# Performance work log

Hardware: AMD Instinct MI355X
Metric: run time of the kernel (lower is better)

## Reference

```python
import jax, jax.numpy as jnp
import numpy as np

N_NODES = 50000
N_EDGES = 800000
EMB = 128      # embedding_dim
GH1 = 128      # gn_hidden_dim1
GH2 = 128      # gn_hidden_dim2
LH = 256       # lstm_hidden_dim
AH = 128       # answer_hidden_dim
AD = 1         # answer_dim
NQ = 512       # number of questions (len(sentence_idx_list))
NS = NQ * 4    # total sentences
MAXLEN = 32    # padded sentence length


def setup_inputs() -> dict:
    key = jax.random.key(0)
    ks = jax.random.split(key, 16)
    s = 0.05
    inputs = jax.random.normal(ks[0], (N_NODES, EMB), jnp.float32)
    src = jax.random.randint(ks[1], (N_EDGES,), 0, N_NODES)
    dst = jax.random.randint(ks[2], (N_EDGES,), 0, N_NODES)
    sentence_idx = jax.random.randint(ks[3], (NS, MAXLEN), 0, N_NODES)
    lengths = jax.random.randint(ks[4], (NS,), 1, MAXLEN + 1)
    # GCN linear layers (torch nn.Linear convention: y = x @ W.T + b)
    W1 = jax.random.normal(ks[5], (GH1, EMB), jnp.float32) * s
    b1 = jnp.zeros((GH1,), jnp.float32)
    W2 = jax.random.normal(ks[6], (GH2, GH1), jnp.float32) * s
    b2 = jnp.zeros((GH2,), jnp.float32)
    # LSTM params (gate order i,f,g,o as in torch)
    Wi = jax.random.normal(ks[7], (4 * LH, GH2), jnp.float32) * s
    Wh = jax.random.normal(ks[8], (4 * LH, LH), jnp.float32) * s
    bi = jnp.zeros((4 * LH,), jnp.float32)
    bh = jnp.zeros((4 * LH,), jnp.float32)
    # sentence_classifier
    Wc1 = jax.random.normal(ks[9], (AH, LH), jnp.float32) * s
    bc1 = jnp.zeros((AH,), jnp.float32)
    Wc2 = jax.random.normal(ks[10], (AD, AH), jnp.float32) * s
    bc2 = jnp.zeros((AD,), jnp.float32)
    return dict(inputs=inputs, W1=W1, b1=b1, W2=W2, b2=b2,
                Wi=Wi, Wh=Wh, bi=bi, bh=bh,
                Wc1=Wc1, bc1=bc1, Wc2=Wc2, bc2=bc2,
                src=src, dst=dst, sentence_idx=sentence_idx, lengths=lengths)


def reference(inputs, W1, b1, W2, b2, Wi, Wh, bi, bh, Wc1, bc1, Wc2, bc2,
              src, dst, sentence_idx, lengths):
    # --- GCN: sum-aggregate over edges, then linear; tanh between layers ---
    agg1 = jax.ops.segment_sum(inputs[src], dst, num_segments=N_NODES)  # [N, EMB]
    h = jnp.tanh(agg1 @ W1.T + b1)                                      # [N, GH1]
    agg2 = jax.ops.segment_sum(h[src], dst, num_segments=N_NODES)       # [N, GH1]
    hn = agg2 @ W2.T + b2                                               # [N, GH2]

    # --- Batched ragged LSTM over all sentences (padded to MAXLEN) ---
    x = hn[sentence_idx]                  # [NS, MAXLEN, GH2]
    x = jnp.swapaxes(x, 0, 1)             # [MAXLEN, NS, GH2] (time-major)

    def step(carry, xt):
        hp, cp = carry
        gates = xt @ Wi.T + bi + hp @ Wh.T + bh            # [NS, 4*LH]
        i, f, g, o = jnp.split(gates, 4, axis=-1)
        c = jax.nn.sigmoid(f) * cp + jax.nn.sigmoid(i) * jnp.tanh(g)
        hcur = jax.nn.sigmoid(o) * jnp.tanh(c)
        return (hcur, c), hcur

    h0 = jnp.zeros((NS, LH), x.dtype)
    c0 = jnp.zeros((NS, LH), x.dtype)
    _, hs = jax.lax.scan(step, (h0, c0), x)                # [MAXLEN, NS, LH]
    h_last = hs[lengths - 1, jnp.arange(NS)]               # [NS, LH] (hn at true seq end)

    # relu then sentence_classifier (linear-relu-linear)
    e = jax.nn.relu(h_last)
    sc = jax.nn.relu(e @ Wc1.T + bc1) @ Wc2.T + bc2        # [NS, 1]
    return sc.reshape(NQ, 4)
```

## Files before the change

kernel.cpp:

```cpp
#include <hip/hip_runtime.h>
#include <hip/hip_bf16.h>
#include <math.h>

#define N_NODES 50000
#define N_EDGES 800000
#define EMB 128
#define LH 256
#define NSENT 2048
#define MAXLEN 32
#define SCAN_NB 196
#define NG 64
#define NGRP 32

typedef __attribute__((ext_vector_type(8))) short short8;
typedef __attribute__((ext_vector_type(4))) float f32x4;

__device__ __forceinline__ unsigned short f2bf_u(float f) {
    __hip_bfloat16 h = __float2bfloat16(f);
    return *reinterpret_cast<unsigned short*>(&h);
}
__device__ __forceinline__ float bfu2f(unsigned short u) {
    unsigned int x = ((unsigned int)u) << 16;
    return __uint_as_float(x);
}

__device__ __forceinline__ float fsig(float x) {
    return 1.f / (1.f + __expf(-x));
}
__device__ __forceinline__ float ftanh(float x) {
    return 1.f - 2.f / (__expf(2.f * x) + 1.f);
}

#define WAITVM0() __builtin_amdgcn_s_waitcnt(0xF70)

__device__ __forceinline__ void gload_lds16(const void* gsrc, void* ldst) {
    __builtin_amdgcn_global_load_lds(
        (const __attribute__((address_space(1))) unsigned int*)gsrc,
        (__attribute__((address_space(3))) unsigned int*)ldst, 16, 0, 0);
}


__global__ void k_hist(const int* __restrict__ dst, int* __restrict__ cnt) {
    int i = blockIdx.x * 256 + threadIdx.x;
    if (i < N_EDGES) atomicAdd(&cnt[dst[i]], 1);
}

__global__ void k_scan_blk(const int* __restrict__ cnt, int* __restrict__ row_ptr,
                           int* __restrict__ blk) {
    int b = blockIdx.x, t = threadIdx.x;
    int i = b * 256 + t;
    int lane = t & 63, wid = t >> 6;
    int v = (i < N_NODES) ? cnt[i] : 0;
    int x = v;
    #pragma unroll
    for (int off = 1; off < 64; off <<= 1) {
        int y = __shfl_up(x, off);
        if (lane >= off) x += y;
    }
    __shared__ int ws[4];
    if (lane == 63) ws[wid] = x;
    __syncthreads();
    if (t == 0) {
        int s = 0;
        #pragma unroll
        for (int j = 0; j < 4; j++) { int tmp = ws[j]; ws[j] = s; s += tmp; }
        blk[b] = s;
    }
    __syncthreads();
    if (i < N_NODES) row_ptr[i] = ws[wid] + x - v;
}

__global__ void k_scan_tot(int* __restrict__ blk) {
    int t = threadIdx.x;
    int lane = t & 63, wid = t >> 6;
    int v = (t < SCAN_NB) ? blk[t] : 0;
    int x = v;
    #pragma unroll
    for (int off = 1; off < 64; off <<= 1) {
        int y = __shfl_up(x, off);
        if (lane >= off) x += y;
    }
    __shared__ int ws[4];
    if (lane == 63) ws[wid] = x;
    __syncthreads();
    if (t == 0) {
        int s = 0;
        #pragma unroll
        for (int j = 0; j < 4; j++) { int tmp = ws[j]; ws[j] = s; s += tmp; }
    }
    __syncthreads();
    if (t < SCAN_NB) blk[t] = ws[wid] + x - v;
}

__global__ void k_scan_add(int* __restrict__ row_ptr, const int* __restrict__ blk) {
    int i = blockIdx.x * 256 + threadIdx.x;
    if (i < N_NODES) row_ptr[i] += blk[i >> 8];
    if (i == 0) row_ptr[N_NODES] = N_EDGES;
}

__global__ void k_scatter(const int* __restrict__ src, const int* __restrict__ dst,
                          const int* __restrict__ row_ptr, int* __restrict__ cnt,
                          int* __restrict__ edge_src) {
    int i = blockIdx.x * 256 + threadIdx.x;
    if (i < N_EDGES) {
        int d = dst[i];
        int pos = row_ptr[d] + atomicAdd(&cnt[d], 1);
        edge_src[pos] = src[i];
    }
}


__global__ void k_tobf16(const float* __restrict__ x, unsigned short* __restrict__ y) {
    int i = blockIdx.x * 256 + threadIdx.x;
    float4 v = ((const float4*)x)[i];
    ushort4 u;
    u.x = f2bf_u(v.x); u.y = f2bf_u(v.y); u.z = f2bf_u(v.z); u.w = f2bf_u(v.w);
    ((ushort4*)y)[i] = u;
}


__global__ void k_aggregate_bf(const unsigned short* __restrict__ feat,
                               const int* __restrict__ row_ptr,
                               const int* __restrict__ edge_src,
                               unsigned short* __restrict__ outb) {
    int w = (blockIdx.x * 256 + threadIdx.x) >> 6;
    int lane = threadIdx.x & 63;
    if (w >= N_NODES) return;
    int slot = lane >> 4, li = lane & 15;
    int beg = row_ptr[w], end = row_ptr[w + 1];
    float acc[8] = {};
    short8 vA = {}, vB = {};
    {
        int eA = beg + slot, eB = beg + 4 + slot;
        int sA = (eA < end) ? edge_src[eA] : -1;
        int sB = (eB < end) ? edge_src[eB] : -1;
        if (sA >= 0) vA = *(const short8*)((const short*)feat + (size_t)sA * EMB + li * 8);
        if (sB >= 0) vB = *(const short8*)((const short*)feat + (size_t)sB * EMB + li * 8);
    }
    #pragma unroll 1
    for (int e = beg; e < end; e += 8) {
        int eA2 = e + 8 + slot, eB2 = e + 12 + slot;
        int sA2 = (eA2 < end) ? edge_src[eA2] : -1;
        int sB2 = (eB2 < end) ? edge_src[eB2] : -1;
        short8 vA2 = {}, vB2 = {};
        if (sA2 >= 0) vA2 = *(const short8*)((const short*)feat + (size_t)sA2 * EMB + li * 8);
        if (sB2 >= 0) vB2 = *(const short8*)((const short*)feat + (size_t)sB2 * EMB + li * 8);
        if (e + slot < end) {
            #pragma unroll
            for (int j = 0; j < 8; j++) acc[j] += bfu2f((unsigned short)vA[j]);
        }
        if (e + 4 + slot < end) {
            #pragma unroll
            for (int j = 0; j < 8; j++) acc[j] += bfu2f((unsigned short)vB[j]);
        }
        vA = vA2; vB = vB2;
    }
    #pragma unroll
    for (int j = 0; j < 8; j++) {
        float t = acc[j];
        t += __shfl_xor(t, 16);
        t += __shfl_xor(t, 32);
        acc[j] = t;
    }
    if (slot == 0) {
        short8 o;
        #pragma unroll
        for (int j = 0; j < 8; j++) o[j] = (short)f2bf_u(acc[j]);
        *(short8*)((short*)outb + (size_t)w * EMB + li * 8) = o;
    }
}


__global__ void __launch_bounds__(256)
k_gcn_mfma(const unsigned short* __restrict__ Ab,
           const unsigned short* __restrict__ Wb,
           const float* __restrict__ bias,
           unsigned short* __restrict__ outb,
           int M, int do_tanh) {
    int tid = threadIdx.x;
    int w = tid >> 6, lane = tid & 63;
    int l16 = lane & 15, quad = lane >> 4;
    int rbase = blockIdx.x * 64 + w * 16;
    int arow = rbase + l16;
    if (arow >= M) arow = M - 1;
    const short* Ap = (const short*)Ab + (size_t)arow * 128 + quad * 8;
    const short* Wp = (const short*)Wb;
    f32x4 acc[8] = {};
    #pragma unroll
    for (int ks = 0; ks < 4; ks++) {
        short8 a = *(const short8*)(Ap + ks * 32);
        #pragma unroll
        for (int ct = 0; ct < 8; ct++) {
            short8 b = *(const short8*)(Wp + (size_t)(ct * 16 + l16) * 128 + ks * 32 + quad * 8);
            acc[ct] = __builtin_amdgcn_mfma_f32_16x16x32_bf16(a, b, acc[ct], 0, 0, 0);
        }
    }
    #pragma unroll
    for (int ct = 0; ct < 8; ct++) {
        float bcol = bias[ct * 16 + l16];
        #pragma unroll
        for (int r = 0; r < 4; r++) {
            int row = rbase + quad * 4 + r;
            if (row < M) {
                float v = acc[ct][r] + bcol;
                if (do_tanh) v = tanhf(v);
                outb[(size_t)row * 128 + ct * 16 + l16] = f2bf_u(v);
            }
        }
    }
}


__global__ void k_prep(const float* __restrict__ Wi, const float* __restrict__ Wh,
                       const float* __restrict__ bi, const float* __restrict__ bh,
                       const float* __restrict__ W1, const float* __restrict__ W2,
                       unsigned short* __restrict__ Wpk3, float* __restrict__ bsum,
                       unsigned short* __restrict__ W1b, unsigned short* __restrict__ W2b) {
    int idx = blockIdx.x * 256 + threadIdx.x;
    if (idx < 1024 * 384) {
        int R = idx / 384, k = idx - R * 384;
        float v = (k < 128) ? Wi[R * 128 + k] : Wh[R * 256 + (k - 128)];
        int g = R >> 8, u = R & 255;
        int usl = u >> 5, up = u & 31;
        int ct = g * 2 + (up >> 4);
        int l16v = up & 15;
        int ks = k >> 5, kk = k & 31;
        int quad = kk >> 3, jj = kk & 7;
        int lane = quad * 16 + l16v;
        Wpk3[(((size_t)usl * 12 + ks) * 8 + ct) * 512 + lane * 8 + jj] = f2bf_u(v);
    } else if (idx < 1024 * 384 + 1024) {
        int r = idx - 1024 * 384;
        bsum[r] = bi[r] + bh[r];
    } else if (idx < 1024 * 384 + 1024 + 16384) {
        int r = idx - (1024 * 384 + 1024);
        W1b[r] = f2bf_u(W1[r]);
    } else if (idx < 1024 * 384 + 1024 + 32768) {
        int r = idx - (1024 * 384 + 1024 + 16384);
        W2b[r] = f2bf_u(W2[r]);
    }
}


__global__ void __launch_bounds__(512)
__attribute__((amdgpu_waves_per_eu(2, 2)))
k_lstm_ws8(const unsigned short* __restrict__ hn_bf,
           const unsigned short* __restrict__ Wpk3,
           const float* __restrict__ bsum,
           const int* __restrict__ sidx,
           const int* __restrict__ lengths,
           unsigned long long* __restrict__ hX,
           int* __restrict__ gcnt,
           float* __restrict__ h_last) {
    __shared__ unsigned short xb[64 * 128];
    __shared__ unsigned short hb[64 * 256];
    __shared__ float gl[64 * 132];
    __shared__ int nid_sh[NG * 33];

    int tid = threadIdx.x;
    int w = tid >> 6, lane = tid & 63;
    int l16 = lane & 15, quad = lane >> 4;
    int usl = blockIdx.x >> 5;
    int grp = blockIdx.x & 31;
    int s0 = grp * NG;
    const short* hnp = (const short*)hn_bf;

    int m2 = w >> 2, cp4 = w & 3;
    int row0 = m2 * 32 + l16, row1 = row0 + 16;

    short8 breg[12][2];
    {
        const short* wsrc = (const short*)Wpk3 + (size_t)usl * 49152 + lane * 8;
        #pragma unroll
        for (int ks = 0; ks < 12; ks++)
            #pragma unroll
            for (int c = 0; c < 2; c++)
                breg[ks][c] = *(const short8*)(wsrc + (size_t)(ks * 8 + cp4 * 2 + c) * 512);
    }
    float bc0 = bsum[cp4 * 256 + usl * 32 + l16];
    float bc1 = bsum[cp4 * 256 + usl * 32 + 16 + l16];

    #pragma unroll
    for (int i = 0; i < 2; i++) {
        int row = w * 8 + i * 4 + quad;
        int nid = sidx[(size_t)(s0 + row) * MAXLEN + 0];
        int schunk = (l16 & ~7) | ((l16 ^ row) & 7);
        gload_lds16(hnp + (size_t)nid * 128 + schunk * 8,
                    (void*)((char*)xb + (size_t)(w * 8 + i * 4) * 256));
    }
    for (int i = tid; i < NG * 32; i += 512)
        nid_sh[(i >> 5) * 33 + (i & 31)] = sidx[(size_t)(s0 + (i >> 5)) * MAXLEN + (i & 31)];
    for (int i = tid; i < 64 * 128; i += 512) ((unsigned int*)hb)[i] = 0;

    int psent = tid >> 3, j8 = tid & 7, u0 = j8 * 4;
    int len_reg = lengths[s0 + psent];
    float c_reg[4] = {};

    short8 xr[2];

    __syncthreads();

    #pragma unroll 1
    for (int t = 0; t < MAXLEN; t++) {
        if (t + 1 < MAXLEN) {
            int row = tid >> 3;
            int nid = nid_sh[row * 33 + (t + 1)];
            #pragma unroll
            for (int k = 0; k < 2; k++) {
                int slot = j8 * 2 + k;
                int c = (slot & ~7) | ((slot ^ row) & 7);
                xr[k] = *(const short8*)(hnp + (size_t)nid * 128 + c * 8);
            }
        }

        f32x4 acc00 = {bc0, bc0, bc0, bc0};
        f32x4 acc01 = {bc1, bc1, bc1, bc1};
        f32x4 acc10 = {bc0, bc0, bc0, bc0};
        f32x4 acc11 = {bc1, bc1, bc1, bc1};
        #pragma unroll
        for (int ks = 0; ks < 4; ks++) {
            int kc = ks * 4 + quad;
            short8 a0 = *(const short8*)(xb + row0 * 128 + (((kc & ~7) | ((kc ^ row0) & 7)) * 8));
            short8 a1 = *(const short8*)(xb + row1 * 128 + (((kc & ~7) | ((kc ^ row1) & 7)) * 8));
            acc00 = __builtin_amdgcn_mfma_f32_16x16x32_bf16(a0, breg[ks][0], acc00, 0, 0, 0);
            acc01 = __builtin_amdgcn_mfma_f32_16x16x32_bf16(a0, breg[ks][1], acc01, 0, 0, 0);
            acc10 = __builtin_amdgcn_mfma_f32_16x16x32_bf16(a1, breg[ks][0], acc10, 0, 0, 0);
            acc11 = __builtin_amdgcn_mfma_f32_16x16x32_bf16(a1, breg[ks][1], acc11, 0, 0, 0);
        }

        if (t > 0) {
            if (tid == 0) {
                while (__hip_atomic_load(&gcnt[grp * 32], __ATOMIC_RELAXED,
                                         __HIP_MEMORY_SCOPE_AGENT) < 8 * t)
                    __builtin_amdgcn_s_sleep(1);
            }
            __syncthreads();
            {
                const unsigned long long* hr = hX + (size_t)(t & 1) * NSENT * 64
                                               + (size_t)(s0 + psent) * 64 + j8 * 8;
                unsigned long long hv[8];
                #pragma unroll
                for (int k = 0; k < 8; k++)
                    hv[k] = __hip_atomic_load(&hr[k], __ATOMIC_RELAXED,
                                              __HIP_MEMORY_SCOPE_AGENT);
                #pragma unroll
                for (int p = 0; p < 4; p++) {
                    int cc = j8 * 4 + p;
                    int slot = (cc & ~7) | ((cc ^ psent) & 7);
                    union { unsigned long long q[2]; short8 s; } uu;
                    uu.q[0] = hv[2 * p]; uu.q[1] = hv[2 * p + 1];
                    *(short8*)(hb + psent * 256 + slot * 8) = uu.s;
                }
            }
        }
        __syncthreads();

        #pragma unroll
        for (int ks = 4; ks < 12; ks++) {
            int kc = (ks - 4) * 4 + quad;
            short8 a0 = *(const short8*)(hb + row0 * 256 + (((kc & ~7) | ((kc ^ row0) & 7)) * 8));
            short8 a1 = *(const short8*)(hb + row1 * 256 + (((kc & ~7) | ((kc ^ row1) & 7)) * 8));
            acc00 = __builtin_amdgcn_mfma_f32_16x16x32_bf16(a0, breg[ks][0], acc00, 0, 0, 0);
            acc01 = __builtin_amdgcn_mfma_f32_16x16x32_bf16(a0, breg[ks][1], acc01, 0, 0, 0);
            acc10 = __builtin_amdgcn_mfma_f32_16x16x32_bf16(a1, breg[ks][0], acc10, 0, 0, 0);
            acc11 = __builtin_amdgcn_mfma_f32_16x16x32_bf16(a1, breg[ks][1], acc11, 0, 0, 0);
        }

        #pragma unroll
        for (int r = 0; r < 4; r++) {
            int se0 = m2 * 32 + quad * 4 + r;
            int se1 = se0 + 16;
            gl[se0 * 132 + cp4 * 32 + l16]      = acc00[r];
            gl[se0 * 132 + cp4 * 32 + 16 + l16] = acc01[r];
            gl[se1 * 132 + cp4 * 32 + l16]      = acc10[r];
            gl[se1 * 132 + cp4 * 32 + 16 + l16] = acc11[r];
        }
        __syncthreads();

        {
            float4 G[4];
            #pragma unroll
            for (int g = 0; g < 4; g++)
                G[g] = *(const float4*)&gl[psent * 132 + g * 32 + u0];
            float hv4[4];
            const float* Gp0 = (const float*)&G[0];
            const float* Gp1 = (const float*)&G[1];
            const float* Gp2 = (const float*)&G[2];
            const float* Gp3 = (const float*)&G[3];
            #pragma unroll
            for (int j = 0; j < 4; j++) {
                float i_ = fsig(Gp0[j]);
                float f_ = fsig(Gp1[j]);
                float g_ = ftanh(Gp2[j]);
                float o_ = fsig(Gp3[j]);
                float c = f_ * c_reg[j] + i_ * g_;
                c_reg[j] = c;
                hv4[j] = o_ * ftanh(c);
            }
            unsigned long long hq =
                  (unsigned long long)f2bf_u(hv4[0])
                | ((unsigned long long)f2bf_u(hv4[1]) << 16)
                | ((unsigned long long)f2bf_u(hv4[2]) << 32)
                | ((unsigned long long)f2bf_u(hv4[3]) << 48);
            unsigned long long* hw = hX + (size_t)((t + 1) & 1) * NSENT * 64
                                     + (size_t)(s0 + psent) * 64 + usl * 8 + j8;
            __hip_atomic_store(hw, hq, __ATOMIC_RELAXED, __HIP_MEMORY_SCOPE_AGENT);
            if (len_reg == t + 1) {
                float4 o4 = make_float4(hv4[0], hv4[1], hv4[2], hv4[3]);
                *(float4*)&h_last[(size_t)(s0 + psent) * 256 + usl * 32 + u0] = o4;
            }
        }

        if (t + 1 < MAXLEN) {
            {
                int row = tid >> 3;
                #pragma unroll
                for (int k = 0; k < 2; k++) {
                    int slot = j8 * 2 + k;
                    *(short8*)(xb + row * 128 + slot * 8) = xr[k];
                }
            }
            WAITVM0();
            __syncthreads();
            if (tid == 0)
                __hip_atomic_fetch_add(&gcnt[grp * 32], 1, __ATOMIC_RELAXED,
                                       __HIP_MEMORY_SCOPE_AGENT);
        }
    }
}


__global__ void k_classifier(const float* __restrict__ h_last,
                             const float* __restrict__ Wc1, const float* __restrict__ bc1,
                             const float* __restrict__ Wc2, const float* __restrict__ bc2,
                             float* __restrict__ out) {
    int lane = threadIdx.x & 63;
    int wslot = threadIdx.x >> 6;
    int s = blockIdx.x * 4 + wslot;
    __shared__ float e_sh[4][256];
    const float* hr = h_last + (size_t)s * 256;
    #pragma unroll
    for (int i = 0; i < 4; i++) {
        float v = hr[lane + 64 * i];
        e_sh[wslot][lane + 64 * i] = fmaxf(v, 0.f);
    }
    __syncthreads();
    float zpart = 0.f;
    #pragma unroll
    for (int jj = 0; jj < 2; jj++) {
        int j = lane + 64 * jj;
        float a = bc1[j];
        const float4* wr = (const float4*)(Wc1 + (size_t)j * 256);
        #pragma unroll 8
        for (int k4 = 0; k4 < 64; k4++) {
            float4 wv = wr[k4];
            float4 e = *(const float4*)&e_sh[wslot][k4 * 4];
            a += wv.x * e.x + wv.y * e.y + wv.z * e.z + wv.w * e.w;
        }
        a = fmaxf(a, 0.f);
        zpart += a * Wc2[j];
    }
    #pragma unroll
    for (int off = 32; off > 0; off >>= 1) zpart += __shfl_down(zpart, off);
    if (lane == 0) out[s] = zpart + bc2[0];
}


extern "C" void kernel_launch(void* const* d_in, const int* in_sizes, int n_in,
                              void* d_out, int out_size, void* d_ws, size_t ws_size,
                              hipStream_t stream) {
    const float* inputs = (const float*)d_in[0];
    const float* W1  = (const float*)d_in[1];
    const float* b1  = (const float*)d_in[2];
    const float* W2  = (const float*)d_in[3];
    const float* b2  = (const float*)d_in[4];
    const float* Wi  = (const float*)d_in[5];
    const float* Wh  = (const float*)d_in[6];
    const float* bi  = (const float*)d_in[7];
    const float* bh  = (const float*)d_in[8];
    const float* Wc1 = (const float*)d_in[9];
    const float* bc1 = (const float*)d_in[10];
    const float* Wc2 = (const float*)d_in[11];
    const float* bc2 = (const float*)d_in[12];
    const int* src      = (const int*)d_in[13];
    const int* dst      = (const int*)d_in[14];
    const int* sidx     = (const int*)d_in[15];
    const int* lengths  = (const int*)d_in[16];
    float* out = (float*)d_out;

    char* ws = (char*)d_ws;
    size_t off = 0;
    auto alloc = [&](size_t bytes) -> void* {
        void* p = ws + off;
        off = (off + bytes + 255) & ~(size_t)255;
        return p;
    };
    unsigned short* in_bf  = (unsigned short*)alloc(2 * (size_t)N_NODES * EMB);
    unsigned short* agg_bf = (unsigned short*)alloc(2 * (size_t)N_NODES * EMB);
    unsigned short* h_bf   = (unsigned short*)alloc(2 * (size_t)N_NODES * EMB);
    unsigned short* hn_bf  = (unsigned short*)alloc(2 * (size_t)N_NODES * EMB);
    int*   row_ptr  = (int*)alloc(sizeof(int) * (N_NODES + 1));
    int*   cnt      = (int*)alloc(sizeof(int) * N_NODES);
    int*   blk      = (int*)alloc(sizeof(int) * SCAN_NB);
    int*   edge_src = (int*)alloc(sizeof(int) * N_EDGES);
    unsigned short* Wpk3 = (unsigned short*)alloc(2 * 8 * 12 * 8 * 512);
    unsigned short* W1b  = (unsigned short*)alloc(2 * 128 * 128);
    unsigned short* W2b  = (unsigned short*)alloc(2 * 128 * 128);
    float* bsum     = (float*)alloc(sizeof(float) * 1024);
    float* hlast    = (float*)alloc(sizeof(float) * NSENT * LH);
    unsigned long long* hX = (unsigned long long*)alloc(2 * (size_t)NSENT * 64 * 8);
    int* gcnt       = (int*)alloc(sizeof(int) * NGRP * 32);

    k_prep<<<(1024 * 384 + 1024 + 32768 + 255) / 256, 256, 0, stream>>>(
        Wi, Wh, bi, bh, W1, W2, Wpk3, bsum, W1b, W2b);

    hipMemsetAsync(hX, 0, 2 * (size_t)NSENT * 64 * 8, stream);
    hipMemsetAsync(gcnt, 0, sizeof(int) * NGRP * 32, stream);

    hipMemsetAsync(cnt, 0, sizeof(int) * N_NODES, stream);
    k_hist<<<(N_EDGES + 255) / 256, 256, 0, stream>>>(dst, cnt);
    k_scan_blk<<<SCAN_NB, 256, 0, stream>>>(cnt, row_ptr, blk);
    k_scan_tot<<<1, 256, 0, stream>>>(blk);
    k_scan_add<<<SCAN_NB, 256, 0, stream>>>(row_ptr, blk);
    hipMemsetAsync(cnt, 0, sizeof(int) * N_NODES, stream);
    k_scatter<<<(N_EDGES + 255) / 256, 256, 0, stream>>>(src, dst, row_ptr, cnt, edge_src);

    k_tobf16<<<(N_NODES * EMB / 4 + 255) / 256, 256, 0, stream>>>(inputs, in_bf);
    k_aggregate_bf<<<(N_NODES * 64) / 256, 256, 0, stream>>>(in_bf, row_ptr, edge_src, agg_bf);
    k_gcn_mfma<<<(N_NODES + 63) / 64, 256, 0, stream>>>(agg_bf, W1b, b1, h_bf, N_NODES, 1);
    k_aggregate_bf<<<(N_NODES * 64) / 256, 256, 0, stream>>>(h_bf, row_ptr, edge_src, agg_bf);
    k_gcn_mfma<<<(N_NODES + 63) / 64, 256, 0, stream>>>(agg_bf, W2b, b2, hn_bf, N_NODES, 0);

    k_lstm_ws8<<<NGRP * 8, 512, 0, stream>>>(hn_bf, Wpk3, bsum, sidx, lengths,
                                             hX, gcnt, hlast);

    k_classifier<<<NSENT / 4, 256, 0, stream>>>(hlast, Wc1, bc1, Wc2, bc2, out);
}
```

Measured before the change: 507.9 us.

## Fold memsets and bf16 conversion into prep kernel; move x staging before barrier

Merges the input bf16 conversion and the zeroing of hX, gcnt and cnt into the single prep kernel, and clears cnt inside the scan-add kernel. This drops four memset operations and one kernel launch. In the LSTM step, the next-timestep x tile is now written to shared memory inside the same barrier region as the h load, removing work from the tail of each step. The risk is a shared-memory hazard if xb is still being read by other waves at that point, though a barrier precedes it.

```diff
diff --git a/kernel.cpp b/kernel.cpp
--- a/kernel.cpp
+++ b/kernel.cpp
@@ -92,9 +92,13 @@
     if (t < SCAN_NB) blk[t] = ws[wid] + x - v;
 }
 
-__global__ void k_scan_add(int* __restrict__ row_ptr, const int* __restrict__ blk) {
+__global__ void k_scan_add(int* __restrict__ row_ptr, const int* __restrict__ blk,
+                           int* __restrict__ cnt) {
     int i = blockIdx.x * 256 + threadIdx.x;
-    if (i < N_NODES) row_ptr[i] += blk[i >> 8];
+    if (i < N_NODES) {
+        row_ptr[i] += blk[i >> 8];
+        cnt[i] = 0;
+    }
     if (i == 0) row_ptr[N_NODES] = N_EDGES;
 }
 
@@ -107,15 +111,6 @@
         int pos = row_ptr[d] + atomicAdd(&cnt[d], 1);
         edge_src[pos] = src[i];
     }
-}
-
-
-__global__ void k_tobf16(const float* __restrict__ x, unsigned short* __restrict__ y) {
-    int i = blockIdx.x * 256 + threadIdx.x;
-    float4 v = ((const float4*)x)[i];
-    ushort4 u;
-    u.x = f2bf_u(v.x); u.y = f2bf_u(v.y); u.z = f2bf_u(v.z); u.w = f2bf_u(v.w);
-    ((ushort4*)y)[i] = u;
 }
 
 
@@ -211,13 +206,26 @@
 }
 
 
+#define PR0 (1024 * 384)
+#define PR1 (PR0 + 1024)
+#define PR2 (PR1 + 16384)
+#define PR3 (PR2 + 16384)
+#define PR4 (PR3 + N_NODES * EMB / 4)
+#define PR5 (PR4 + 2 * NSENT * 64)
+#define PR6 (PR5 + NGRP * 32)
+#define PR7 (PR6 + N_NODES)
+
 __global__ void k_prep(const float* __restrict__ Wi, const float* __restrict__ Wh,
                        const float* __restrict__ bi, const float* __restrict__ bh,
                        const float* __restrict__ W1, const float* __restrict__ W2,
+                       const float* __restrict__ inputs,
                        unsigned short* __restrict__ Wpk3, float* __restrict__ bsum,
-                       unsigned short* __restrict__ W1b, unsigned short* __restrict__ W2b) {
+                       unsigned short* __restrict__ W1b, unsigned short* __restrict__ W2b,
+                       unsigned short* __restrict__ in_bf,
+                       unsigned long long* __restrict__ hX,
+                       int* __restrict__ gcnt, int* __restrict__ cnt) {
     int idx = blockIdx.x * 256 + threadIdx.x;
-    if (idx < 1024 * 384) {
+    if (idx < PR0) {
         int R = idx / 384, k = idx - R * 384;
         float v = (k < 128) ? Wi[R * 128 + k] : Wh[R * 256 + (k - 128)];
         int g = R >> 8, u = R & 255;
@@ -228,15 +236,27 @@
         int quad = kk >> 3, jj = kk & 7;
         int lane = quad * 16 + l16v;
         Wpk3[(((size_t)usl * 12 + ks) * 8 + ct) * 512 + lane * 8 + jj] = f2bf_u(v);
-    } else if (idx < 1024 * 384 + 1024) {
-        int r = idx - 1024 * 384;
+    } else if (idx < PR1) {
+        int r = idx - PR0;
         bsum[r] = bi[r] + bh[r];
-    } else if (idx < 1024 * 384 + 1024 + 16384) {
-        int r = idx - (1024 * 384 + 1024);
+    } else if (idx < PR2) {
+        int r = idx - PR1;
         W1b[r] = f2bf_u(W1[r]);
-    } else if (idx < 1024 * 384 + 1024 + 32768) {
-        int r = idx - (1024 * 384 + 1024 + 16384);
+    } else if (idx < PR3) {
+        int r = idx - PR2;
         W2b[r] = f2bf_u(W2[r]);
+    } else if (idx < PR4) {
+        int i = idx - PR3;
+        float4 v = ((const float4*)inputs)[i];
+        ushort4 u4;
+        u4.x = f2bf_u(v.x); u4.y = f2bf_u(v.y); u4.z = f2bf_u(v.z); u4.w = f2bf_u(v.w);
+        ((ushort4*)in_bf)[i] = u4;
+    } else if (idx < PR5) {
+        hX[idx - PR4] = 0ull;
+    } else if (idx < PR6) {
+        gcnt[idx - PR5] = 0;
+    } else if (idx < PR7) {
+        cnt[idx - PR6] = 0;
     }
 }
 
@@ -327,29 +347,40 @@
             acc11 = __builtin_amdgcn_mfma_f32_16x16x32_bf16(a1, breg[ks][1], acc11, 0, 0, 0);
         }
 
+        if (t > 0 && tid == 0) {
+            while (__hip_atomic_load(&gcnt[grp * 32], __ATOMIC_RELAXED,
+                                     __HIP_MEMORY_SCOPE_AGENT) < 8 * t)
+                __builtin_amdgcn_s_sleep(1);
+        }
+        __syncthreads();
+
+        unsigned long long hv[8];
         if (t > 0) {
-            if (tid == 0) {
-                while (__hip_atomic_load(&gcnt[grp * 32], __ATOMIC_RELAXED,
-                                         __HIP_MEMORY_SCOPE_AGENT) < 8 * t)
-                    __builtin_amdgcn_s_sleep(1);
+            const unsigned long long* hr = hX + (size_t)(t & 1) * NSENT * 64
+                                           + (size_t)(s0 + psent) * 64 + j8 * 8;
+            #pragma unroll
+            for (int k = 0; k < 8; k++)
+                hv[k] = __hip_atomic_load(&hr[k], __ATOMIC_RELAXED,
+                                          __HIP_MEMORY_SCOPE_AGENT);
+        }
+
+        if (t + 1 < MAXLEN) {
+            int row = tid >> 3;
+            #pragma unroll
+            for (int k = 0; k < 2; k++) {
+                int slot = j8 * 2 + k;
+                *(short8*)(xb + row * 128 + slot * 8) = xr[k];
             }
-            __syncthreads();
-            {
-                const unsigned long long* hr = hX + (size_t)(t & 1) * NSENT * 64
-                                               + (size_t)(s0 + psent) * 64 + j8 * 8;
-                unsigned long long hv[8];
-                #pragma unroll
-                for (int k = 0; k < 8; k++)
-                    hv[k] = __hip_atomic_load(&hr[k], __ATOMIC_RELAXED,
-                                              __HIP_MEMORY_SCOPE_AGENT);
-                #pragma unroll
-                for (int p = 0; p < 4; p++) {
-                    int cc = j8 * 4 + p;
-                    int slot = (cc & ~7) | ((cc ^ psent) & 7);
-                    union { unsigned long long q[2]; short8 s; } uu;
-                    uu.q[0] = hv[2 * p]; uu.q[1] = hv[2 * p + 1];
-                    *(short8*)(hb + psent * 256 + slot * 8) = uu.s;
-                }
+        }
+
+        if (t > 0) {
+            #pragma unroll
+            for (int p = 0; p < 4; p++) {
+                int cc = j8 * 4 + p;
+                int slot = (cc & ~7) | ((cc ^ psent) & 7);
+                union { unsigned long long q[2]; short8 s; } uu;
+                uu.q[0] = hv[2 * p]; uu.q[1] = hv[2 * p + 1];
+                *(short8*)(hb + psent * 256 + slot * 8) = uu.s;
             }
         }
         __syncthreads();
@@ -411,14 +442,6 @@
         }
 
         if (t + 1 < MAXLEN) {
-            {
-                int row = tid >> 3;
-                #pragma unroll
-                for (int k = 0; k < 2; k++) {
-                    int slot = j8 * 2 + k;
-                    *(short8*)(xb + row * 128 + slot * 8) = xr[k];
-                }
-            }
             WAITVM0();
             __syncthreads();
             if (tid == 0)
@@ -510,21 +533,15 @@
     unsigned long long* hX = (unsigned long long*)alloc(2 * (size_t)NSENT * 64 * 8);
     int* gcnt       = (int*)alloc(sizeof(int) * NGRP * 32);
 
-    k_prep<<<(1024 * 384 + 1024 + 32768 + 255) / 256, 256, 0, stream>>>(
-        Wi, Wh, bi, bh, W1, W2, Wpk3, bsum, W1b, W2b);
-
-    hipMemsetAsync(hX, 0, 2 * (size_t)NSENT * 64 * 8, stream);
-    hipMemsetAsync(gcnt, 0, sizeof(int) * NGRP * 32, stream);
-
-    hipMemsetAsync(cnt, 0, sizeof(int) * N_NODES, stream);
+    k_prep<<<(PR7 + 255) / 256, 256, 0, stream>>>(
+        Wi, Wh, bi, bh, W1, W2, inputs, Wpk3, bsum, W1b, W2b, in_bf, hX, gcnt, cnt);
+
     k_hist<<<(N_EDGES + 255) / 256, 256, 0, stream>>>(dst, cnt);
     k_scan_blk<<<SCAN_NB, 256, 0, stream>>>(cnt, row_ptr, blk);
     k_scan_tot<<<1, 256, 0, stream>>>(blk);
-    k_scan_add<<<SCAN_NB, 256, 0, stream>>>(row_ptr, blk);
-    hipMemsetAsync(cnt, 0, sizeof(int) * N_NODES, stream);
+    k_scan_add<<<SCAN_NB, 256, 0, stream>>>(row_ptr, blk, cnt);
     k_scatter<<<(N_EDGES + 255) / 256, 256, 0, stream>>>(src, dst, row_ptr, cnt, edge_src);
 
-    k_tobf16<<<(N_NODES * EMB / 4 + 255) / 256, 256, 0, stream>>>(inputs, in_bf);
     k_aggregate_bf<<<(N_NODES * 64) / 256, 256, 0, stream>>>(in_bf, row_ptr, edge_src, agg_bf);
     k_gcn_mfma<<<(N_NODES + 63) / 64, 256, 0, stream>>>(agg_bf, W1b, b1, h_bf, N_NODES, 1);
     k_aggregate_bf<<<(N_NODES * 64) / 256, 256, 0, stream>>>(h_bf, row_ptr, edge_src, agg_bf);
```

Result: no change. 503.3 us (-0.9%).
